# Performance work log

Hardware: AMD Instinct MI355X
Metric: run time of the kernel (lower is better)

Reference implementation:

```python
import jax, jax.numpy as jnp
import numpy as np

N, H, F, E, K = 4096, 512, 2048, 8, 2  # tokens, hidden, ffn(=4H), experts, top_k


def setup_inputs() -> dict:
    key = jax.random.key(0)
    ks = jax.random.split(key, 7)
    def w(k, shape, fan_in):
        return jax.random.normal(k, shape, dtype=jnp.float32) * (fan_in ** -0.5)
    return {
        "x": jax.random.normal(ks[0], (N, H), dtype=jnp.float32),
        "W_in": w(ks[1], (H, H), H),          # input_proj.weight  [out,in]
        "W_router": w(ks[2], (E, H), H),      # router.gate.weight [E,H]
        "W_gate": w(ks[3], (E, F, H), H),     # per-expert gate_proj.weight
        "W_up": w(ks[4], (E, F, H), H),       # per-expert up_proj.weight
        "W_down": w(ks[5], (E, H, F), F),     # per-expert down_proj.weight
        "W_out": w(ks[6], (H, H), H),         # output_proj.weight
    }


def reference(x, W_in, W_router, W_gate, W_up, W_down, W_out):
    h = x @ W_in.T                                  # [N,H] input_proj
    logits = h @ W_router.T                         # [N,E]
    # route_mode='balanced' and world_size==1 -> expert_bias is None
    probs = jax.nn.softmax(logits, axis=-1)
    top_w, top_i = jax.lax.top_k(probs, K)          # [N,K]
    top_w = jax.nn.softmax(top_w, axis=-1)          # renormalize over top-k

    # per-token combine weight for each expert: [N,E]
    onehot = jax.nn.one_hot(top_i, E, dtype=h.dtype)      # [N,K,E]
    combine_w = jnp.einsum('nk,nke->ne', top_w, onehot)

    def expert(wg, wu, wd):
        # SwiGLU FFN: down( silu(gate(h)) * up(h) )
        return (jax.nn.silu(h @ wg.T) * (h @ wu.T)) @ wd.T  # [N,H]

    expert_out = jax.vmap(expert)(W_gate, W_up, W_down)     # [E,N,H]
    combined = jnp.einsum('ne,enh->nh', combine_w, expert_out)
    return combined @ W_out.T                                # output_proj
```

## Files before the change

kernel.cpp:

```cpp
#include <hip/hip_runtime.h>

typedef unsigned short u16;
typedef unsigned int u32;
typedef short bf16x8 __attribute__((ext_vector_type(8)));
typedef float f32x4 __attribute__((ext_vector_type(4)));

#define AS1 __attribute__((address_space(1)))
#define AS3 __attribute__((address_space(3)))

#define NTOK 4096
#define HDIM 512
#define FDIM 2048
#define NEXP 8
#define NASSIGN (NTOK * 2)
#define NPAD (NASSIGN + NEXP * 128)
#define RBMAX 128

__device__ __forceinline__ void g2l16(const void* g, void* l) {
  __builtin_amdgcn_global_load_lds((const AS1 u32*)g, (AS3 u32*)l, 16, 0, 0);
}
__device__ __forceinline__ u16 f2bf(float f) {
  u32 u = __float_as_uint(f);
  u = (u + 0x7FFFu + ((u >> 16) & 1u)) >> 16;
  return (u16)u;
}
__device__ __forceinline__ float bf2f(u16 h) { return __uint_as_float(((u32)h) << 16); }

#define WAITV6() asm volatile("s_waitcnt vmcnt(6)" ::: "memory")
#define WAITV4() asm volatile("s_waitcnt vmcnt(4)" ::: "memory")
#define WAITV0() asm volatile("s_waitcnt vmcnt(0)" ::: "memory")
#define BAR() __builtin_amdgcn_s_barrier()
#define VMBAR() do { WAITV0(); BAR(); } while (0)

__global__ __launch_bounds__(256) void cvtall_kernel(
    const float* __restrict__ x, const float* __restrict__ Wi, const float* __restrict__ Wo,
    const float* __restrict__ Wg, const float* __restrict__ Wu, const float* __restrict__ Wd,
    u16* __restrict__ xb, u16* __restrict__ Wib, u16* __restrict__ Wob,
    u16* __restrict__ Wgb, u16* __restrict__ Wub, u16* __restrict__ Wdb) {
  const int gid = blockIdx.x * 256 + threadIdx.x;
  const int S = 6784 * 256;
#pragma unroll
  for (int k = 0; k < 4; ++k) {
    const int i = gid + k * S;
    const float* s; u16* d; int o;
    if (i < 524288) { s = x; d = xb; o = i; }
    else if (i < 589824) { s = Wi; d = Wib; o = i - 524288; }
    else if (i < 655360) { s = Wo; d = Wob; o = i - 589824; }
    else if (i < 2752512) { s = Wg; d = Wgb; o = i - 655360; }
    else if (i < 4849664) { s = Wu; d = Wub; o = i - 2752512; }
    else { s = Wd; d = Wdb; o = i - 4849664; }
    const float4 v = ((const float4*)s)[o];
    ushort4 t; t.x = f2bf(v.x); t.y = f2bf(v.y); t.z = f2bf(v.z); t.w = f2bf(v.w);
    ((ushort4*)d)[o] = t;
  }
}

__global__ __launch_bounds__(256) void wreff_kernel(
    const float* __restrict__ Wr, const float* __restrict__ Wi, double* __restrict__ wre) {
  const int t = blockIdx.x * 256 + threadIdx.x;
  const int e = t >> 9, k = t & 511;
  const float* wr = Wr + e * HDIM;
  double a = 0.0;
  for (int j = 0; j < HDIM; j += 8) {
#pragma unroll
    for (int u = 0; u < 8; ++u) a += (double)wr[j + u] * (double)Wi[(j + u) * HDIM + k];
  }
  wre[t] = a;
}

__global__ __launch_bounds__(256) void router_kernel(
    const float* __restrict__ x, const double* __restrict__ wre,
    int* __restrict__ idx, float* __restrict__ wts) {
  __shared__ double lw[NEXP * HDIM];
  for (int i = threadIdx.x; i < NEXP * HDIM; i += 256) lw[i] = wre[i];
  __syncthreads();
  const int n = blockIdx.x * 256 + threadIdx.x;
  const float* xr = x + (size_t)n * HDIM;
  double acc[NEXP] = {};
  for (int k4 = 0; k4 < HDIM / 4; ++k4) {
    const float4 xv = ((const float4*)xr)[k4];
    const float xc[4] = {xv.x, xv.y, xv.z, xv.w};
#pragma unroll
    for (int c = 0; c < 4; ++c) {
      const double xd = (double)xc[c];
#pragma unroll
      for (int e = 0; e < NEXP; ++e) acc[e] += xd * lw[e * HDIM + k4 * 4 + c];
    }
  }
  double mx = acc[0];
#pragma unroll
  for (int e = 1; e < NEXP; ++e) mx = acc[e] > mx ? acc[e] : mx;
  double p[NEXP], se = 0.0;
#pragma unroll
  for (int e = 0; e < NEXP; ++e) { p[e] = exp(acc[e] - mx); se += p[e]; }
  const double inv = 1.0 / se;
#pragma unroll
  for (int e = 0; e < NEXP; ++e) p[e] *= inv;
  int i0 = 0; double b0 = p[0];
#pragma unroll
  for (int e = 1; e < NEXP; ++e) if (p[e] > b0) { b0 = p[e]; i0 = e; }
  int i1 = -1; double b1 = -1.0;
#pragma unroll
  for (int e = 0; e < NEXP; ++e) if (e != i0 && p[e] > b1) { b1 = p[e]; i1 = e; }
  const double e0 = exp(b0), e1 = exp(b1);
  idx[2 * n] = i0; idx[2 * n + 1] = i1;
  wts[2 * n] = (float)(e0 / (e0 + e1));
  wts[2 * n + 1] = (float)(e1 / (e0 + e1));
}

__global__ void assign_kernel(const int* __restrict__ idx, int* __restrict__ tok,
                              int* __restrict__ pos, int* __restrict__ rbe,
                              int* __restrict__ rbp, int* __restrict__ nrb) {
  __shared__ int cnt[NEXP], cur[NEXP];
  const int tid = threadIdx.x;
  if (tid < NEXP) cnt[tid] = 0;
  __syncthreads();
  for (int a = tid; a < NASSIGN; a += 256) atomicAdd(&cnt[idx[a]], 1);
  __syncthreads();
  if (tid == 0) {
    int o = 0, n = 0;
    for (int e = 0; e < NEXP; ++e) {
      cur[e] = o;
      const int nb = (cnt[e] + 127) >> 7;
      for (int i = 0; i < nb; ++i) { rbe[n] = e; rbp[n] = o + i * 128; ++n; }
      o += nb * 128;
    }
    nrb[0] = n;
  }
  __syncthreads();
  for (int p = tid; p < NPAD; p += 256) tok[p] = 0;
  __syncthreads();
  for (int a = tid; a < NASSIGN; a += 256) {
    const int e = idx[a];
    const int q = atomicAdd(&cur[e], 1);
    tok[q] = a >> 1;
    pos[a] = q;
  }
}

template <int SB, int NT>
__device__ __forceinline__ void gemm128_body(
    const u16* __restrict__ A, const u16* __restrict__ B, void* __restrict__ C,
    int m0, int n0, int N, int K, u16* sm, int tid) {
  u16 *lA0 = sm, *lA1 = sm + 8192, *lB0 = sm + 16384, *lB1 = sm + 24576;
  const int w = tid >> 6, l = tid & 63;
  const int wm = (w >> 2) * 64, wn = (w & 3) * 32;
  const int lm = l & 15, lk = (l >> 4) * 8, xr = (l & 7) << 3;
  const int sr = l >> 3, sc = ((l & 7) ^ sr) * 8;
  const u16* As = A + (size_t)(m0 + w * 8 + sr) * K + sc;
  const u16* Bs = B + (size_t)(n0 + w * 8 + sr) * K + sc;
  f32x4 acc[4][2] = {};
  auto STG = [&](u16* dA, u16* dB, int kt) {
    g2l16(As + kt, dA + w * 512);
    g2l16(As + (size_t)64 * K + kt, dA + 4096 + w * 512);
    g2l16(Bs + kt, dB + w * 512);
    g2l16(Bs + (size_t)64 * K + kt, dB + 4096 + w * 512);
  };
  auto CMP = [&](const u16* a_, const u16* b_) {
#pragma unroll
    for (int kk = 0; kk < 2; ++kk) {
      const int ko = (kk * 32 + lk) ^ xr;
      bf16x8 af[4], bf[2];
#pragma unroll
      for (int i = 0; i < 4; ++i) af[i] = *(const bf16x8*)(a_ + (wm + i * 16 + lm) * 64 + ko);
#pragma unroll
      for (int j = 0; j < 2; ++j) bf[j] = *(const bf16x8*)(b_ + (wn + j * 16 + lm) * 64 + ko);
#pragma unroll
      for (int i = 0; i < 4; ++i)
#pragma unroll
        for (int j = 0; j < 2; ++j)
          acc[i][j] = __builtin_amdgcn_mfma_f32_16x16x32_bf16(af[i], bf[j], acc[i][j], 0, 0, 0);
    }
  };
  STG(lA0, lB0, 0);
  VMBAR();
  for (int t = 0; t < NT; t += 2) {
    if (t + 1 < NT) STG(lA1, lB1, (t + 1) * 64);
    CMP(lA0, lB0);
    VMBAR();
    if (t + 2 < NT) STG(lA0, lB0, (t + 2) * 64);
    CMP(lA1, lB1);
    VMBAR();
  }
  const int cr = (l >> 4) * 4, cc = lm;
#pragma unroll
  for (int i = 0; i < 4; ++i)
#pragma unroll
    for (int j = 0; j < 2; ++j)
#pragma unroll
      for (int r = 0; r < 4; ++r) {
        const size_t o = (size_t)(m0 + wm + i * 16 + cr + r) * N + n0 + wn + j * 16 + cc;
        if (SB) ((u16*)C)[o] = f2bf(acc[i][j][r]);
        else ((float*)C)[o] = acc[i][j][r];
      }
}

__global__ __launch_bounds__(512, 2) void ingemm_kernel(
    const u16* __restrict__ xb, const u16* __restrict__ Wib, u16* __restrict__ hb) {
  __shared__ __align__(16) u16 sm[32768];
  gemm128_body<1, 8>(xb, Wib, hb, blockIdx.y * 128, blockIdx.x * 128, HDIM, HDIM, sm, threadIdx.x);
}

__global__ __launch_bounds__(512, 2) void outgemm_kernel(
    const u16* __restrict__ cb, const u16* __restrict__ Wob, float* __restrict__ out) {
  __shared__ __align__(16) u16 sm[32768];
  gemm128_body<0, 8>(cb, Wob, out, blockIdx.y * 128, blockIdx.x * 128, HDIM, HDIM, sm, threadIdx.x);
}

__global__ __launch_bounds__(512, 2) void gateup_kernel(
    const u16* __restrict__ hb, const u16* __restrict__ Wg, const u16* __restrict__ Wu,
    u16* __restrict__ act, const int* __restrict__ tok, const int* __restrict__ rbe,
    const int* __restrict__ rbp, const int* __restrict__ nrb) {
  const int rb = blockIdx.y;
  if (rb >= nrb[0]) return;
  __shared__ __align__(16) u16 sm[73728];
  const int e = rbe[rb], p0 = rbp[rb], n0 = blockIdx.x * 128;
  const int tid = threadIdx.x, w = tid >> 6, l = tid & 63;
  const int wm = (w >> 2) * 64, wn = (w & 3) * 32;
  const int lm = l & 15, lk = (l >> 4) * 8, xr = (l & 7) << 3;
  const int sr = l >> 3, sc = ((l & 7) ^ sr) * 8;
  const u16* A0 = hb + (size_t)tok[p0 + w * 8 + sr] * HDIM + sc;
  const u16* A1 = hb + (size_t)tok[p0 + 64 + w * 8 + sr] * HDIM + sc;
  const u16* G0 = Wg + (size_t)e * FDIM * HDIM + (size_t)(n0 + w * 8 + sr) * HDIM + sc;
  const u16* G1 = G0 + (size_t)64 * HDIM;
  const u16* U0 = Wu + (size_t)e * FDIM * HDIM + (size_t)(n0 + w * 8 + sr) * HDIM + sc;
  const u16* U1 = U0 + (size_t)64 * HDIM;
  f32x4 ag[4][2] = {}, au[4][2] = {};
  auto STG = [&](int b, int kt) {
    u16* d = sm + b * 24576;
    g2l16(A0 + kt, d + w * 512);
    g2l16(A1 + kt, d + 4096 + w * 512);
    g2l16(G0 + kt, d + 8192 + w * 512);
    g2l16(G1 + kt, d + 12288 + w * 512);
    g2l16(U0 + kt, d + 16384 + w * 512);
    g2l16(U1 + kt, d + 20480 + w * 512);
  };
  auto CMP = [&](int b) {
    const u16* a_ = sm + b * 24576;
    const u16* g_ = a_ + 8192;
    const u16* u_ = a_ + 16384;
#pragma unroll
    for (int kk = 0; kk < 2; ++kk) {
      const int ko = (kk * 32 + lk) ^ xr;
      bf16x8 af[4], gf[2], uf[2];
#pragma unroll
      for (int i = 0; i < 4; ++i) af[i] = *(const bf16x8*)(a_ + (wm + i * 16 + lm) * 64 + ko);
#pragma unroll
      for (int j = 0; j < 2; ++j) {
        gf[j] = *(const bf16x8*)(g_ + (wn + j * 16 + lm) * 64 + ko);
        uf[j] = *(const bf16x8*)(u_ + (wn + j * 16 + lm) * 64 + ko);
      }
#pragma unroll
      for (int i = 0; i < 4; ++i)
#pragma unroll
        for (int j = 0; j < 2; ++j) {
          ag[i][j] = __builtin_amdgcn_mfma_f32_16x16x32_bf16(af[i], gf[j], ag[i][j], 0, 0, 0);
          au[i][j] = __builtin_amdgcn_mfma_f32_16x16x32_bf16(af[i], uf[j], au[i][j], 0, 0, 0);
        }
    }
  };
  STG(0, 0); STG(1, 64);
  WAITV6(); BAR();
#pragma unroll
  for (int t = 0; t < 8; ++t) {
    if (t + 2 < 8) STG((t + 2) % 3, (t + 2) * 64);
    CMP(t % 3);
    if (t + 2 < 8) WAITV6(); else WAITV0();
    BAR();
  }
  const int cr = (l >> 4) * 4, cc = lm;
#pragma unroll
  for (int i = 0; i < 4; ++i)
#pragma unroll
    for (int j = 0; j < 2; ++j)
#pragma unroll
      for (int r = 0; r < 4; ++r) {
        const float g = ag[i][j][r], u = au[i][j][r];
        const float s = g / (1.0f + __expf(-g));
        act[(size_t)(p0 + wm + i * 16 + cr + r) * FDIM + n0 + wn + j * 16 + cc] = f2bf(s * u);
      }
}

__global__ __launch_bounds__(512, 2) void down_kernel(
    const u16* __restrict__ act, const u16* __restrict__ Wd, u16* __restrict__ dwn,
    const int* __restrict__ rbe, const int* __restrict__ rbp, const int* __restrict__ nrb) {
  const int rb = blockIdx.y;
  if (rb >= nrb[0]) return;
  __shared__ __align__(16) u16 sm[49152];
  const int e = rbe[rb], p0 = rbp[rb], n0 = blockIdx.x * 128;
  const int tid = threadIdx.x, w = tid >> 6, l = tid & 63;
  const int g = w >> 2;
  const int wm = ((w >> 1) & 1) * 64, wn = (w & 1) * 64;
  const int lm = l & 15, lk = (l >> 4) * 8, xr = (l & 7) << 3;
  const int ko = (g * 32 + lk) ^ xr;
  const int sr = l >> 3, sc = ((l & 7) ^ sr) * 8;
  const u16* As = act + (size_t)(p0 + w * 8 + sr) * FDIM + sc;
  const u16* Bs = Wd + (size_t)e * HDIM * FDIM + (size_t)(n0 + w * 8 + sr) * FDIM + sc;
  f32x4 acc[4][4] = {};
  auto STG = [&](int b, int kt) {
    u16* d = sm + b * 16384;
    g2l16(As + kt, d + w * 512);
    g2l16(As + (size_t)64 * FDIM + kt, d + 4096 + w * 512);
    g2l16(Bs + kt, d + 8192 + w * 512);
    g2l16(Bs + (size_t)64 * FDIM + kt, d + 12288 + w * 512);
  };
  auto CMP = [&](int b) {
    const u16* a_ = sm + b * 16384;
    const u16* b_ = a_ + 8192;
    bf16x8 af[4], bf[4];
#pragma unroll
    for (int i = 0; i < 4; ++i) af[i] = *(const bf16x8*)(a_ + (wm + i * 16 + lm) * 64 + ko);
#pragma unroll
    for (int j = 0; j < 4; ++j) bf[j] = *(const bf16x8*)(b_ + (wn + j * 16 + lm) * 64 + ko);
#pragma unroll
    for (int i = 0; i < 4; ++i)
#pragma unroll
      for (int j = 0; j < 4; ++j)
        acc[i][j] = __builtin_amdgcn_mfma_f32_16x16x32_bf16(af[i], bf[j], acc[i][j], 0, 0, 0);
  };
  STG(0, 0); STG(1, 64);
  WAITV4(); BAR();
#pragma unroll
  for (int t = 0; t < 32; ++t) {
    if (t + 2 < 32) STG((t + 2) % 3, (t + 2) * 64);
    CMP(t % 3);
    if (t + 2 < 32) WAITV4(); else WAITV0();
    BAR();
  }
  asm volatile("s_waitcnt lgkmcnt(0)" ::: "memory");
  __builtin_amdgcn_sched_barrier(0);
  BAR();
  float* red = (float*)sm;
  if (g == 1) {
#pragma unroll
    for (int i = 0; i < 4; ++i)
#pragma unroll
      for (int j = 0; j < 4; ++j)
        *(f32x4*)&red[(w & 3) * 4096 + (i * 4 + j) * 256 + l * 4] = acc[i][j];
  }
  BAR();
  if (g == 0) {
    const int cr = (l >> 4) * 4, cc = lm;
#pragma unroll
    for (int i = 0; i < 4; ++i)
#pragma unroll
      for (int j = 0; j < 4; ++j) {
        const f32x4 o = *(const f32x4*)&red[w * 4096 + (i * 4 + j) * 256 + l * 4];
        const f32x4 s = acc[i][j] + o;
#pragma unroll
        for (int r = 0; r < 4; ++r)
          dwn[(size_t)(p0 + wm + i * 16 + cr + r) * HDIM + n0 + wn + j * 16 + cc] = f2bf(s[r]);
      }
  }
}

__global__ void combine_kernel(const u16* __restrict__ dwn, const int* __restrict__ pos,
                               const float* __restrict__ wts, u16* __restrict__ cb) {
  const int n = blockIdx.x, t = threadIdx.x;
  const int p0 = pos[2 * n], p1 = pos[2 * n + 1];
  const float w0 = wts[2 * n], w1 = wts[2 * n + 1];
  const ushort4 a = ((const ushort4*)(dwn + (size_t)p0 * HDIM))[t];
  const ushort4 b = ((const ushort4*)(dwn + (size_t)p1 * HDIM))[t];
  ushort4 o;
  o.x = f2bf(w0 * bf2f(a.x) + w1 * bf2f(b.x));
  o.y = f2bf(w0 * bf2f(a.y) + w1 * bf2f(b.y));
  o.z = f2bf(w0 * bf2f(a.z) + w1 * bf2f(b.z));
  o.w = f2bf(w0 * bf2f(a.w) + w1 * bf2f(b.w));
  ((ushort4*)(cb + (size_t)n * HDIM))[t] = o;
}

extern "C" void kernel_launch(void* const* d_in, const int* in_sizes, int n_in,
                              void* d_out, int out_size, void* d_ws, size_t ws_size,
                              hipStream_t stream) {
  const float* x  = (const float*)d_in[0];
  const float* Wi = (const float*)d_in[1];
  const float* Wr = (const float*)d_in[2];
  const float* Wg = (const float*)d_in[3];
  const float* Wu = (const float*)d_in[4];
  const float* Wd = (const float*)d_in[5];
  const float* Wo = (const float*)d_in[6];
  float* out = (float*)d_out;

  char* ws = (char*)d_ws;
  size_t off = 0;
  auto alloc = [&](size_t bytes) -> void* {
    off = (off + 255) & ~(size_t)255;
    void* p = ws + off;
    off += bytes;
    return p;
  };
  u16* xb  = (u16*)alloc((size_t)NTOK * HDIM * 2);
  u16* hb  = (u16*)alloc((size_t)NTOK * HDIM * 2);
  u16* cb  = (u16*)alloc((size_t)NTOK * HDIM * 2);
  u16* Wib = (u16*)alloc((size_t)HDIM * HDIM * 2);
  u16* Wob = (u16*)alloc((size_t)HDIM * HDIM * 2);
  u16* Wgb = (u16*)alloc((size_t)NEXP * FDIM * HDIM * 2);
  u16* Wub = (u16*)alloc((size_t)NEXP * FDIM * HDIM * 2);
  u16* Wdb = (u16*)alloc((size_t)NEXP * HDIM * FDIM * 2);
  u16* actb = (u16*)alloc((size_t)NPAD * FDIM * 2);
  u16* dwn = (u16*)alloc((size_t)NPAD * HDIM * 2);
  double* wre = (double*)alloc((size_t)NEXP * HDIM * 8);
  int* idx = (int*)alloc((size_t)NASSIGN * 4);
  float* wts = (float*)alloc((size_t)NASSIGN * 4);
  int* tok = (int*)alloc((size_t)NPAD * 4);
  int* pos = (int*)alloc((size_t)NASSIGN * 4);
  int* rbe = (int*)alloc((size_t)RBMAX * 4);
  int* rbp = (int*)alloc((size_t)RBMAX * 4);
  int* nrb = (int*)alloc(256);

  cvtall_kernel<<<6784, 256, 0, stream>>>(x, Wi, Wo, Wg, Wu, Wd, xb, Wib, Wob, Wgb, Wub, Wdb);
  wreff_kernel<<<16, 256, 0, stream>>>(Wr, Wi, wre);
  router_kernel<<<16, 256, 0, stream>>>(x, wre, idx, wts);
  assign_kernel<<<1, 256, 0, stream>>>(idx, tok, pos, rbe, rbp, nrb);
  ingemm_kernel<<<dim3(4, 32), 512, 0, stream>>>(xb, Wib, hb);
  gateup_kernel<<<dim3(16, 72), 512, 0, stream>>>(hb, Wgb, Wub, actb, tok, rbe, rbp, nrb);
  down_kernel<<<dim3(4, 72), 512, 0, stream>>>(actb, Wdb, dwn, rbe, rbp, nrb);
  combine_kernel<<<NTOK, 128, 0, stream>>>(dwn, pos, wts, cb);
  outgemm_kernel<<<dim3(4, 32), 512, 0, stream>>>(cb, Wob, out);
}
```

Baseline: 218.2 us.

## Fuse combine into output GEMM, restructure conversion, tune router and wreff

```diff
diff --git a/kernel.cpp b/kernel.cpp
--- a/kernel.cpp
+++ b/kernel.cpp
@@ -1,4 +1,5 @@
 #include <hip/hip_runtime.h>
+#include <hip/hip_bf16.h>
 
 typedef unsigned short u16;
 typedef unsigned int u32;
@@ -25,11 +26,28 @@
   return (u16)u;
 }
 __device__ __forceinline__ float bf2f(u16 h) { return __uint_as_float(((u32)h) << 16); }
+__device__ __forceinline__ u32 pkbf(float a, float b) {
+  __hip_bfloat162 h = __float22bfloat162_rn(float2{a, b});
+  u32 r;
+  __builtin_memcpy(&r, &h, 4);
+  return r;
+}
+__device__ __forceinline__ int4 pk8(const float4 a, const float4 b) {
+  int4 r;
+  r.x = (int)pkbf(a.x, a.y); r.y = (int)pkbf(a.z, a.w);
+  r.z = (int)pkbf(b.x, b.y); r.w = (int)pkbf(b.z, b.w);
+  return r;
+}
 
 #define WAITV6() asm volatile("s_waitcnt vmcnt(6)" ::: "memory")
 #define WAITV4() asm volatile("s_waitcnt vmcnt(4)" ::: "memory")
+#define WAITV2() asm volatile("s_waitcnt vmcnt(2)" ::: "memory")
 #define WAITV0() asm volatile("s_waitcnt vmcnt(0)" ::: "memory")
+#define LGKM0() asm volatile("s_waitcnt lgkmcnt(0)" ::: "memory")
 #define BAR() __builtin_amdgcn_s_barrier()
+#define SCB() __builtin_amdgcn_sched_barrier(0)
+#define PRIO1() __builtin_amdgcn_s_setprio(1)
+#define PRIO0() __builtin_amdgcn_s_setprio(0)
 #define VMBAR() do { WAITV0(); BAR(); } while (0)
 
 __global__ __launch_bounds__(256) void cvtall_kernel(
@@ -37,22 +55,26 @@
     const float* __restrict__ Wg, const float* __restrict__ Wu, const float* __restrict__ Wd,
     u16* __restrict__ xb, u16* __restrict__ Wib, u16* __restrict__ Wob,
     u16* __restrict__ Wgb, u16* __restrict__ Wub, u16* __restrict__ Wdb) {
-  const int gid = blockIdx.x * 256 + threadIdx.x;
-  const int S = 6784 * 256;
-#pragma unroll
-  for (int k = 0; k < 4; ++k) {
-    const int i = gid + k * S;
-    const float* s; u16* d; int o;
-    if (i < 524288) { s = x; d = xb; o = i; }
-    else if (i < 589824) { s = Wi; d = Wib; o = i - 524288; }
-    else if (i < 655360) { s = Wo; d = Wob; o = i - 589824; }
-    else if (i < 2752512) { s = Wg; d = Wgb; o = i - 655360; }
-    else if (i < 4849664) { s = Wu; d = Wub; o = i - 2752512; }
-    else { s = Wd; d = Wdb; o = i - 4849664; }
-    const float4 v = ((const float4*)s)[o];
-    ushort4 t; t.x = f2bf(v.x); t.y = f2bf(v.y); t.z = f2bf(v.z); t.w = f2bf(v.w);
-    ((ushort4*)d)[o] = t;
-  }
+  const int c = blockIdx.x, tid = threadIdx.x;
+  const float* s; u16* d; int cs;
+  if (c < 128) { s = x; d = xb; cs = 0; }
+  else if (c < 144) { s = Wi; d = Wib; cs = 128; }
+  else if (c < 160) { s = Wo; d = Wob; cs = 144; }
+  else if (c < 672) { s = Wg; d = Wgb; cs = 160; }
+  else if (c < 1184) { s = Wu; d = Wub; cs = 672; }
+  else { s = Wd; d = Wdb; cs = 1184; }
+  const size_t base = (size_t)(c - cs) * 16384 + (size_t)tid * 8;
+  const float* sp = s + base;
+  u16* dp = d + base;
+  float4 a[16];
+#pragma unroll
+  for (int j = 0; j < 8; ++j) {
+    a[2 * j] = *(const float4*)(sp + j * 2048);
+    a[2 * j + 1] = *(const float4*)(sp + j * 2048 + 4);
+  }
+#pragma unroll
+  for (int j = 0; j < 8; ++j)
+    *(int4*)(dp + j * 2048) = pk8(a[2 * j], a[2 * j + 1]);
 }
 
 __global__ __launch_bounds__(256) void wreff_kernel(
@@ -60,21 +82,23 @@
   const int t = blockIdx.x * 256 + threadIdx.x;
   const int e = t >> 9, k = t & 511;
   const float* wr = Wr + e * HDIM;
-  double a = 0.0;
-  for (int j = 0; j < HDIM; j += 8) {
-#pragma unroll
-    for (int u = 0; u < 8; ++u) a += (double)wr[j + u] * (double)Wi[(j + u) * HDIM + k];
-  }
-  wre[t] = a;
-}
-
-__global__ __launch_bounds__(256) void router_kernel(
+  double a0 = 0.0, a1 = 0.0, a2 = 0.0, a3 = 0.0;
+  for (int j = 0; j < HDIM; j += 4) {
+    a0 += (double)wr[j + 0] * (double)Wi[(j + 0) * HDIM + k];
+    a1 += (double)wr[j + 1] * (double)Wi[(j + 1) * HDIM + k];
+    a2 += (double)wr[j + 2] * (double)Wi[(j + 2) * HDIM + k];
+    a3 += (double)wr[j + 3] * (double)Wi[(j + 3) * HDIM + k];
+  }
+  wre[t] = (a0 + a1) + (a2 + a3);
+}
+
+__global__ __launch_bounds__(128) void router_kernel(
     const float* __restrict__ x, const double* __restrict__ wre,
     int* __restrict__ idx, float* __restrict__ wts) {
   __shared__ double lw[NEXP * HDIM];
-  for (int i = threadIdx.x; i < NEXP * HDIM; i += 256) lw[i] = wre[i];
+  for (int i = threadIdx.x; i < NEXP * HDIM; i += 128) lw[i] = wre[i];
   __syncthreads();
-  const int n = blockIdx.x * 256 + threadIdx.x;
+  const int n = blockIdx.x * 128 + threadIdx.x;
   const float* xr = x + (size_t)n * HDIM;
   double acc[NEXP] = {};
   for (int k4 = 0; k4 < HDIM / 4; ++k4) {
@@ -165,11 +189,13 @@
       for (int i = 0; i < 4; ++i) af[i] = *(const bf16x8*)(a_ + (wm + i * 16 + lm) * 64 + ko);
 #pragma unroll
       for (int j = 0; j < 2; ++j) bf[j] = *(const bf16x8*)(b_ + (wn + j * 16 + lm) * 64 + ko);
+      PRIO1();
 #pragma unroll
       for (int i = 0; i < 4; ++i)
 #pragma unroll
         for (int j = 0; j < 2; ++j)
           acc[i][j] = __builtin_amdgcn_mfma_f32_16x16x32_bf16(af[i], bf[j], acc[i][j], 0, 0, 0);
+      PRIO0();
     }
   };
   STG(lA0, lB0, 0);
@@ -202,9 +228,82 @@
 }
 
 __global__ __launch_bounds__(512, 2) void outgemm_kernel(
-    const u16* __restrict__ cb, const u16* __restrict__ Wob, float* __restrict__ out) {
+    const u16* __restrict__ dwn, const u16* __restrict__ Wob, const int* __restrict__ pos,
+    const float* __restrict__ wts, float* __restrict__ out) {
   __shared__ __align__(16) u16 sm[32768];
-  gemm128_body<0, 8>(cb, Wob, out, blockIdx.y * 128, blockIdx.x * 128, HDIM, HDIM, sm, threadIdx.x);
+  const int m0 = blockIdx.y * 128, n0 = blockIdx.x * 128;
+  const int tid = threadIdx.x, w = tid >> 6, l = tid & 63;
+  const int wm = (w >> 2) * 64, wn = (w & 3) * 32;
+  const int lm = l & 15, lk = (l >> 4) * 8, xr = (l & 7) << 3;
+  const int lr = l >> 3, c8 = l & 7;
+  const int sc = (c8 ^ lr) * 8;
+  const int t0 = m0 + w * 8 + lr, t1 = t0 + 64;
+  const int p00 = pos[2 * t0], p01 = pos[2 * t0 + 1];
+  const int p10 = pos[2 * t1], p11 = pos[2 * t1 + 1];
+  const float w00 = wts[2 * t0], w01 = wts[2 * t0 + 1];
+  const float w10 = wts[2 * t1], w11 = wts[2 * t1 + 1];
+  const u16* A00 = dwn + (size_t)p00 * HDIM + c8 * 8;
+  const u16* A01 = dwn + (size_t)p01 * HDIM + c8 * 8;
+  const u16* A10 = dwn + (size_t)p10 * HDIM + c8 * 8;
+  const u16* A11 = dwn + (size_t)p11 * HDIM + c8 * 8;
+  const u16* Bs = Wob + (size_t)(n0 + w * 8 + lr) * HDIM + sc;
+  f32x4 acc[4][2] = {};
+  bf16x8 a00, a01, a10, a11;
+  auto ALOAD = [&](int kt) {
+    a00 = *(const bf16x8*)(A00 + kt); a01 = *(const bf16x8*)(A01 + kt);
+    a10 = *(const bf16x8*)(A10 + kt); a11 = *(const bf16x8*)(A11 + kt);
+  };
+  auto AWRITE = [&](u16* st) {
+    bf16x8 r0, r1;
+#pragma unroll
+    for (int q = 0; q < 8; ++q) {
+      r0[q] = (short)f2bf(w00 * bf2f((u16)a00[q]) + w01 * bf2f((u16)a01[q]));
+      r1[q] = (short)f2bf(w10 * bf2f((u16)a10[q]) + w11 * bf2f((u16)a11[q]));
+    }
+    *(bf16x8*)(st + (w * 8 + lr) * 64 + sc) = r0;
+    *(bf16x8*)(st + (64 + w * 8 + lr) * 64 + sc) = r1;
+  };
+  auto STGB = [&](u16* st, int kt) {
+    g2l16(Bs + kt, st + 8192 + w * 512);
+    g2l16(Bs + (size_t)64 * HDIM + kt, st + 8192 + 4096 + w * 512);
+  };
+  auto CMP = [&](const u16* a_, const u16* b_) {
+#pragma unroll
+    for (int kk = 0; kk < 2; ++kk) {
+      const int ko = (kk * 32 + lk) ^ xr;
+      bf16x8 af[4], bf[2];
+#pragma unroll
+      for (int i = 0; i < 4; ++i) af[i] = *(const bf16x8*)(a_ + (wm + i * 16 + lm) * 64 + ko);
+#pragma unroll
+      for (int j = 0; j < 2; ++j) bf[j] = *(const bf16x8*)(b_ + (wn + j * 16 + lm) * 64 + ko);
+      PRIO1();
+#pragma unroll
+      for (int i = 0; i < 4; ++i)
+#pragma unroll
+        for (int j = 0; j < 2; ++j)
+          acc[i][j] = __builtin_amdgcn_mfma_f32_16x16x32_bf16(af[i], bf[j], acc[i][j], 0, 0, 0);
+      PRIO0();
+    }
+  };
+  ALOAD(0); SCB(); STGB(sm, 0);
+  WAITV2(); AWRITE(sm);
+  WAITV0(); LGKM0(); BAR(); SCB();
+  for (int t = 0; t < 8; ++t) {
+    u16* bu = sm + (t & 1) * 16384;
+    u16* bn = sm + ((t + 1) & 1) * 16384;
+    if (t < 7) { ALOAD((t + 1) * 64); SCB(); STGB(bn, (t + 1) * 64); }
+    CMP(bu, bu + 8192);
+    if (t < 7) { WAITV2(); AWRITE(bn); WAITV0(); }
+    LGKM0(); BAR(); SCB();
+  }
+  const int cr = (l >> 4) * 4, cc = lm;
+#pragma unroll
+  for (int i = 0; i < 4; ++i)
+#pragma unroll
+    for (int j = 0; j < 2; ++j)
+#pragma unroll
+      for (int r = 0; r < 4; ++r)
+        out[(size_t)(m0 + wm + i * 16 + cr + r) * HDIM + n0 + wn + j * 16 + cc] = acc[i][j][r];
 }
 
 __global__ __launch_bounds__(512, 2) void gateup_kernel(
@@ -327,8 +426,8 @@
     if (t + 2 < 32) WAITV4(); else WAITV0();
     BAR();
   }
-  asm volatile("s_waitcnt lgkmcnt(0)" ::: "memory");
-  __builtin_amdgcn_sched_barrier(0);
+  LGKM0();
+  SCB();
   BAR();
   float* red = (float*)sm;
   if (g == 1) {
@@ -352,21 +451,6 @@
           dwn[(size_t)(p0 + wm + i * 16 + cr + r) * HDIM + n0 + wn + j * 16 + cc] = f2bf(s[r]);
       }
   }
-}
-
-__global__ void combine_kernel(const u16* __restrict__ dwn, const int* __restrict__ pos,
-                               const float* __restrict__ wts, u16* __restrict__ cb) {
-  const int n = blockIdx.x, t = threadIdx.x;
-  const int p0 = pos[2 * n], p1 = pos[2 * n + 1];
-  const float w0 = wts[2 * n], w1 = wts[2 * n + 1];
-  const ushort4 a = ((const ushort4*)(dwn + (size_t)p0 * HDIM))[t];
-  const ushort4 b = ((const ushort4*)(dwn + (size_t)p1 * HDIM))[t];
-  ushort4 o;
-  o.x = f2bf(w0 * bf2f(a.x) + w1 * bf2f(b.x));
-  o.y = f2bf(w0 * bf2f(a.y) + w1 * bf2f(b.y));
-  o.z = f2bf(w0 * bf2f(a.z) + w1 * bf2f(b.z));
-  o.w = f2bf(w0 * bf2f(a.w) + w1 * bf2f(b.w));
-  ((ushort4*)(cb + (size_t)n * HDIM))[t] = o;
 }
 
 extern "C" void kernel_launch(void* const* d_in, const int* in_sizes, int n_in,
@@ -389,16 +473,15 @@
     off += bytes;
     return p;
   };
-  u16* xb  = (u16*)alloc((size_t)NTOK * HDIM * 2);
-  u16* hb  = (u16*)alloc((size_t)NTOK * HDIM * 2);
-  u16* cb  = (u16*)alloc((size_t)NTOK * HDIM * 2);
-  u16* Wib = (u16*)alloc((size_t)HDIM * HDIM * 2);
-  u16* Wob = (u16*)alloc((size_t)HDIM * HDIM * 2);
-  u16* Wgb = (u16*)alloc((size_t)NEXP * FDIM * HDIM * 2);
-  u16* Wub = (u16*)alloc((size_t)NEXP * FDIM * HDIM * 2);
-  u16* Wdb = (u16*)alloc((size_t)NEXP * HDIM * FDIM * 2);
+  u16* xb   = (u16*)alloc((size_t)NTOK * HDIM * 2);
+  u16* hb   = (u16*)alloc((size_t)NTOK * HDIM * 2);
+  u16* Wib  = (u16*)alloc((size_t)HDIM * HDIM * 2);
+  u16* Wob  = (u16*)alloc((size_t)HDIM * HDIM * 2);
+  u16* Wgb  = (u16*)alloc((size_t)NEXP * FDIM * HDIM * 2);
+  u16* Wub  = (u16*)alloc((size_t)NEXP * FDIM * HDIM * 2);
+  u16* Wdb  = (u16*)alloc((size_t)NEXP * HDIM * FDIM * 2);
   u16* actb = (u16*)alloc((size_t)NPAD * FDIM * 2);
-  u16* dwn = (u16*)alloc((size_t)NPAD * HDIM * 2);
+  u16* dwn  = (u16*)alloc((size_t)NPAD * HDIM * 2);
   double* wre = (double*)alloc((size_t)NEXP * HDIM * 8);
   int* idx = (int*)alloc((size_t)NASSIGN * 4);
   float* wts = (float*)alloc((size_t)NASSIGN * 4);
@@ -408,13 +491,12 @@
   int* rbp = (int*)alloc((size_t)RBMAX * 4);
   int* nrb = (int*)alloc(256);
 
-  cvtall_kernel<<<6784, 256, 0, stream>>>(x, Wi, Wo, Wg, Wu, Wd, xb, Wib, Wob, Wgb, Wub, Wdb);
+  cvtall_kernel<<<1696, 256, 0, stream>>>(x, Wi, Wo, Wg, Wu, Wd, xb, Wib, Wob, Wgb, Wub, Wdb);
   wreff_kernel<<<16, 256, 0, stream>>>(Wr, Wi, wre);
-  router_kernel<<<16, 256, 0, stream>>>(x, wre, idx, wts);
+  router_kernel<<<32, 128, 0, stream>>>(x, wre, idx, wts);
   assign_kernel<<<1, 256, 0, stream>>>(idx, tok, pos, rbe, rbp, nrb);
   ingemm_kernel<<<dim3(4, 32), 512, 0, stream>>>(xb, Wib, hb);
   gateup_kernel<<<dim3(16, 72), 512, 0, stream>>>(hb, Wgb, Wub, actb, tok, rbe, rbp, nrb);
   down_kernel<<<dim3(4, 72), 512, 0, stream>>>(actb, Wdb, dwn, rbe, rbp, nrb);
-  combine_kernel<<<NTOK, 128, 0, stream>>>(dwn, pos, wts, cb);
-  outgemm_kernel<<<dim3(4, 32), 512, 0, stream>>>(cb, Wob, out);
-}
+  outgemm_kernel<<<dim3(4, 32), 512, 0, stream>>>(dwn, Wob, pos, wts, out);
+}
```

After: 226.6 us. +3.9%, slower.

## Retile GEMMs to 128x64 blocks, rework conversion, router and down kernels

Applied to the files above, without the earlier changes.

```diff
diff --git a/kernel.cpp b/kernel.cpp
--- a/kernel.cpp
+++ b/kernel.cpp
@@ -1,4 +1,5 @@
 #include <hip/hip_runtime.h>
+#include <hip/hip_bf16.h>
 
 typedef unsigned short u16;
 typedef unsigned int u32;
@@ -25,11 +26,26 @@
   return (u16)u;
 }
 __device__ __forceinline__ float bf2f(u16 h) { return __uint_as_float(((u32)h) << 16); }
+__device__ __forceinline__ u32 pkbf(float a, float b) {
+  __hip_bfloat162 h = __float22bfloat162_rn(float2{a, b});
+  u32 r;
+  __builtin_memcpy(&r, &h, 4);
+  return r;
+}
+__device__ __forceinline__ int4 pk8(const float4 a, const float4 b) {
+  int4 r;
+  r.x = (int)pkbf(a.x, a.y); r.y = (int)pkbf(a.z, a.w);
+  r.z = (int)pkbf(b.x, b.y); r.w = (int)pkbf(b.z, b.w);
+  return r;
+}
 
 #define WAITV6() asm volatile("s_waitcnt vmcnt(6)" ::: "memory")
-#define WAITV4() asm volatile("s_waitcnt vmcnt(4)" ::: "memory")
 #define WAITV0() asm volatile("s_waitcnt vmcnt(0)" ::: "memory")
+#define LGKM0() asm volatile("s_waitcnt lgkmcnt(0)" ::: "memory")
 #define BAR() __builtin_amdgcn_s_barrier()
+#define SCB() __builtin_amdgcn_sched_barrier(0)
+#define PRIO1() __builtin_amdgcn_s_setprio(1)
+#define PRIO0() __builtin_amdgcn_s_setprio(0)
 #define VMBAR() do { WAITV0(); BAR(); } while (0)
 
 __global__ __launch_bounds__(256) void cvtall_kernel(
@@ -37,22 +53,26 @@
     const float* __restrict__ Wg, const float* __restrict__ Wu, const float* __restrict__ Wd,
     u16* __restrict__ xb, u16* __restrict__ Wib, u16* __restrict__ Wob,
     u16* __restrict__ Wgb, u16* __restrict__ Wub, u16* __restrict__ Wdb) {
-  const int gid = blockIdx.x * 256 + threadIdx.x;
-  const int S = 6784 * 256;
-#pragma unroll
-  for (int k = 0; k < 4; ++k) {
-    const int i = gid + k * S;
-    const float* s; u16* d; int o;
-    if (i < 524288) { s = x; d = xb; o = i; }
-    else if (i < 589824) { s = Wi; d = Wib; o = i - 524288; }
-    else if (i < 655360) { s = Wo; d = Wob; o = i - 589824; }
-    else if (i < 2752512) { s = Wg; d = Wgb; o = i - 655360; }
-    else if (i < 4849664) { s = Wu; d = Wub; o = i - 2752512; }
-    else { s = Wd; d = Wdb; o = i - 4849664; }
-    const float4 v = ((const float4*)s)[o];
-    ushort4 t; t.x = f2bf(v.x); t.y = f2bf(v.y); t.z = f2bf(v.z); t.w = f2bf(v.w);
-    ((ushort4*)d)[o] = t;
-  }
+  const int c = blockIdx.x, tid = threadIdx.x;
+  const float* s; u16* d; int cs;
+  if (c < 128) { s = x; d = xb; cs = 0; }
+  else if (c < 144) { s = Wi; d = Wib; cs = 128; }
+  else if (c < 160) { s = Wo; d = Wob; cs = 144; }
+  else if (c < 672) { s = Wg; d = Wgb; cs = 160; }
+  else if (c < 1184) { s = Wu; d = Wub; cs = 672; }
+  else { s = Wd; d = Wdb; cs = 1184; }
+  const size_t base = (size_t)(c - cs) * 16384 + (size_t)tid * 8;
+  const float* sp = s + base;
+  u16* dp = d + base;
+  float4 a[16];
+#pragma unroll
+  for (int j = 0; j < 8; ++j) {
+    a[2 * j] = *(const float4*)(sp + j * 2048);
+    a[2 * j + 1] = *(const float4*)(sp + j * 2048 + 4);
+  }
+#pragma unroll
+  for (int j = 0; j < 8; ++j)
+    *(int4*)(dp + j * 2048) = pk8(a[2 * j], a[2 * j + 1]);
 }
 
 __global__ __launch_bounds__(256) void wreff_kernel(
@@ -60,21 +80,23 @@
   const int t = blockIdx.x * 256 + threadIdx.x;
   const int e = t >> 9, k = t & 511;
   const float* wr = Wr + e * HDIM;
-  double a = 0.0;
-  for (int j = 0; j < HDIM; j += 8) {
-#pragma unroll
-    for (int u = 0; u < 8; ++u) a += (double)wr[j + u] * (double)Wi[(j + u) * HDIM + k];
-  }
-  wre[t] = a;
-}
-
-__global__ __launch_bounds__(256) void router_kernel(
+  double a0 = 0.0, a1 = 0.0, a2 = 0.0, a3 = 0.0;
+  for (int j = 0; j < HDIM; j += 4) {
+    a0 += (double)wr[j + 0] * (double)Wi[(j + 0) * HDIM + k];
+    a1 += (double)wr[j + 1] * (double)Wi[(j + 1) * HDIM + k];
+    a2 += (double)wr[j + 2] * (double)Wi[(j + 2) * HDIM + k];
+    a3 += (double)wr[j + 3] * (double)Wi[(j + 3) * HDIM + k];
+  }
+  wre[t] = (a0 + a1) + (a2 + a3);
+}
+
+__global__ __launch_bounds__(128) void router_kernel(
     const float* __restrict__ x, const double* __restrict__ wre,
     int* __restrict__ idx, float* __restrict__ wts) {
   __shared__ double lw[NEXP * HDIM];
-  for (int i = threadIdx.x; i < NEXP * HDIM; i += 256) lw[i] = wre[i];
-  __syncthreads();
-  const int n = blockIdx.x * 256 + threadIdx.x;
+  for (int i = threadIdx.x; i < NEXP * HDIM; i += 128) lw[i] = wre[i];
+  __syncthreads();
+  const int n = blockIdx.x * 128 + threadIdx.x;
   const float* xr = x + (size_t)n * HDIM;
   double acc[NEXP] = {};
   for (int k4 = 0; k4 < HDIM / 4; ++k4) {
@@ -132,29 +154,30 @@
   __syncthreads();
   for (int a = tid; a < NASSIGN; a += 256) {
     const int e = idx[a];
-    const int q = atomicAdd(&cur[e], 1);
+    const int q = atomicAdd(&cur[a >= 0 ? e : 0], 1);
     tok[q] = a >> 1;
     pos[a] = q;
   }
 }
 
 template <int SB, int NT>
-__device__ __forceinline__ void gemm128_body(
+__device__ __forceinline__ void gemm64_body(
     const u16* __restrict__ A, const u16* __restrict__ B, void* __restrict__ C,
-    int m0, int n0, int N, int K, u16* sm, int tid) {
-  u16 *lA0 = sm, *lA1 = sm + 8192, *lB0 = sm + 16384, *lB1 = sm + 24576;
+    int n0, int N, int K, u16* sm, int tid) {
+  u16 *l0 = sm, *l1 = sm + 12288;
   const int w = tid >> 6, l = tid & 63;
-  const int wm = (w >> 2) * 64, wn = (w & 3) * 32;
+  const int wm = (w >> 1) * 64, wn = (w & 1) * 32;
   const int lm = l & 15, lk = (l >> 4) * 8, xr = (l & 7) << 3;
   const int sr = l >> 3, sc = ((l & 7) ^ sr) * 8;
-  const u16* As = A + (size_t)(m0 + w * 8 + sr) * K + sc;
+  const u16* As = A + (size_t)(w * 8 + sr) * K + sc;
   const u16* Bs = B + (size_t)(n0 + w * 8 + sr) * K + sc;
   f32x4 acc[4][2] = {};
-  auto STG = [&](u16* dA, u16* dB, int kt) {
-    g2l16(As + kt, dA + w * 512);
-    g2l16(As + (size_t)64 * K + kt, dA + 4096 + w * 512);
-    g2l16(Bs + kt, dB + w * 512);
-    g2l16(Bs + (size_t)64 * K + kt, dB + 4096 + w * 512);
+  auto STG = [&](u16* d, int kt) {
+#pragma unroll
+    for (int c = 0; c < 4; ++c) g2l16(As + (size_t)(c * 32) * K + kt, d + c * 2048 + w * 512);
+#pragma unroll
+    for (int c = 0; c < 2; ++c)
+      g2l16(Bs + (size_t)(c * 32) * K + kt, d + 8192 + c * 2048 + w * 512);
   };
   auto CMP = [&](const u16* a_, const u16* b_) {
 #pragma unroll
@@ -165,21 +188,23 @@
       for (int i = 0; i < 4; ++i) af[i] = *(const bf16x8*)(a_ + (wm + i * 16 + lm) * 64 + ko);
 #pragma unroll
       for (int j = 0; j < 2; ++j) bf[j] = *(const bf16x8*)(b_ + (wn + j * 16 + lm) * 64 + ko);
+      PRIO1();
 #pragma unroll
       for (int i = 0; i < 4; ++i)
 #pragma unroll
         for (int j = 0; j < 2; ++j)
           acc[i][j] = __builtin_amdgcn_mfma_f32_16x16x32_bf16(af[i], bf[j], acc[i][j], 0, 0, 0);
+      PRIO0();
     }
   };
-  STG(lA0, lB0, 0);
+  STG(l0, 0);
   VMBAR();
   for (int t = 0; t < NT; t += 2) {
-    if (t + 1 < NT) STG(lA1, lB1, (t + 1) * 64);
-    CMP(lA0, lB0);
+    if (t + 1 < NT) STG(l1, (t + 1) * 64);
+    CMP(l0, l0 + 8192);
     VMBAR();
-    if (t + 2 < NT) STG(lA0, lB0, (t + 2) * 64);
-    CMP(lA1, lB1);
+    if (t + 2 < NT) STG(l0, (t + 2) * 64);
+    CMP(l1, l1 + 8192);
     VMBAR();
   }
   const int cr = (l >> 4) * 4, cc = lm;
@@ -189,22 +214,37 @@
     for (int j = 0; j < 2; ++j)
 #pragma unroll
       for (int r = 0; r < 4; ++r) {
-        const size_t o = (size_t)(m0 + wm + i * 16 + cr + r) * N + n0 + wn + j * 16 + cc;
+        const size_t o = (size_t)(wm + i * 16 + cr + r) * N + n0 + wn + j * 16 + cc;
         if (SB) ((u16*)C)[o] = f2bf(acc[i][j][r]);
         else ((float*)C)[o] = acc[i][j][r];
       }
 }
 
-__global__ __launch_bounds__(512, 2) void ingemm_kernel(
+__global__ __launch_bounds__(256, 3) void ingemm_kernel(
     const u16* __restrict__ xb, const u16* __restrict__ Wib, u16* __restrict__ hb) {
-  __shared__ __align__(16) u16 sm[32768];
-  gemm128_body<1, 8>(xb, Wib, hb, blockIdx.y * 128, blockIdx.x * 128, HDIM, HDIM, sm, threadIdx.x);
-}
-
-__global__ __launch_bounds__(512, 2) void outgemm_kernel(
+  __shared__ __align__(16) u16 sm[24576];
+  const int m0 = blockIdx.y * 128;
+  gemm64_body<1, 8>(xb + (size_t)m0 * HDIM, Wib, hb + (size_t)m0 * HDIM,
+                    blockIdx.x * 64, HDIM, HDIM, sm, threadIdx.x);
+}
+
+__global__ __launch_bounds__(256, 3) void outgemm_kernel(
     const u16* __restrict__ cb, const u16* __restrict__ Wob, float* __restrict__ out) {
-  __shared__ __align__(16) u16 sm[32768];
-  gemm128_body<0, 8>(cb, Wob, out, blockIdx.y * 128, blockIdx.x * 128, HDIM, HDIM, sm, threadIdx.x);
+  __shared__ __align__(16) u16 sm[24576];
+  const int m0 = blockIdx.y * 128;
+  gemm64_body<0, 8>(cb + (size_t)m0 * HDIM, Wob, out + (size_t)m0 * HDIM,
+                    blockIdx.x * 64, HDIM, HDIM, sm, threadIdx.x);
+}
+
+__global__ __launch_bounds__(256, 3) void down_kernel(
+    const u16* __restrict__ act, const u16* __restrict__ Wd, u16* __restrict__ dwn,
+    const int* __restrict__ rbe, const int* __restrict__ rbp, const int* __restrict__ nrb) {
+  const int rb = blockIdx.y;
+  if (rb >= nrb[0]) return;
+  __shared__ __align__(16) u16 sm[24576];
+  const int e = rbe[rb], p0 = rbp[rb];
+  gemm64_body<1, 32>(act + (size_t)p0 * FDIM, Wd + (size_t)e * HDIM * FDIM,
+                     dwn + (size_t)p0 * HDIM, blockIdx.x * 64, HDIM, FDIM, sm, threadIdx.x);
 }
 
 __global__ __launch_bounds__(512, 2) void gateup_kernel(
@@ -281,79 +321,6 @@
       }
 }
 
-__global__ __launch_bounds__(512, 2) void down_kernel(
-    const u16* __restrict__ act, const u16* __restrict__ Wd, u16* __restrict__ dwn,
-    const int* __restrict__ rbe, const int* __restrict__ rbp, const int* __restrict__ nrb) {
-  const int rb = blockIdx.y;
-  if (rb >= nrb[0]) return;
-  __shared__ __align__(16) u16 sm[49152];
-  const int e = rbe[rb], p0 = rbp[rb], n0 = blockIdx.x * 128;
-  const int tid = threadIdx.x, w = tid >> 6, l = tid & 63;
-  const int g = w >> 2;
-  const int wm = ((w >> 1) & 1) * 64, wn = (w & 1) * 64;
-  const int lm = l & 15, lk = (l >> 4) * 8, xr = (l & 7) << 3;
-  const int ko = (g * 32 + lk) ^ xr;
-  const int sr = l >> 3, sc = ((l & 7) ^ sr) * 8;
-  const u16* As = act + (size_t)(p0 + w * 8 + sr) * FDIM + sc;
-  const u16* Bs = Wd + (size_t)e * HDIM * FDIM + (size_t)(n0 + w * 8 + sr) * FDIM + sc;
-  f32x4 acc[4][4] = {};
-  auto STG = [&](int b, int kt) {
-    u16* d = sm + b * 16384;
-    g2l16(As + kt, d + w * 512);
-    g2l16(As + (size_t)64 * FDIM + kt, d + 4096 + w * 512);
-    g2l16(Bs + kt, d + 8192 + w * 512);
-    g2l16(Bs + (size_t)64 * FDIM + kt, d + 12288 + w * 512);
-  };
-  auto CMP = [&](int b) {
-    const u16* a_ = sm + b * 16384;
-    const u16* b_ = a_ + 8192;
-    bf16x8 af[4], bf[4];
-#pragma unroll
-    for (int i = 0; i < 4; ++i) af[i] = *(const bf16x8*)(a_ + (wm + i * 16 + lm) * 64 + ko);
-#pragma unroll
-    for (int j = 0; j < 4; ++j) bf[j] = *(const bf16x8*)(b_ + (wn + j * 16 + lm) * 64 + ko);
-#pragma unroll
-    for (int i = 0; i < 4; ++i)
-#pragma unroll
-      for (int j = 0; j < 4; ++j)
-        acc[i][j] = __builtin_amdgcn_mfma_f32_16x16x32_bf16(af[i], bf[j], acc[i][j], 0, 0, 0);
-  };
-  STG(0, 0); STG(1, 64);
-  WAITV4(); BAR();
-#pragma unroll
-  for (int t = 0; t < 32; ++t) {
-    if (t + 2 < 32) STG((t + 2) % 3, (t + 2) * 64);
-    CMP(t % 3);
-    if (t + 2 < 32) WAITV4(); else WAITV0();
-    BAR();
-  }
-  asm volatile("s_waitcnt lgkmcnt(0)" ::: "memory");
-  __builtin_amdgcn_sched_barrier(0);
-  BAR();
-  float* red = (float*)sm;
-  if (g == 1) {
-#pragma unroll
-    for (int i = 0; i < 4; ++i)
-#pragma unroll
-      for (int j = 0; j < 4; ++j)
-        *(f32x4*)&red[(w & 3) * 4096 + (i * 4 + j) * 256 + l * 4] = acc[i][j];
-  }
-  BAR();
-  if (g == 0) {
-    const int cr = (l >> 4) * 4, cc = lm;
-#pragma unroll
-    for (int i = 0; i < 4; ++i)
-#pragma unroll
-      for (int j = 0; j < 4; ++j) {
-        const f32x4 o = *(const f32x4*)&red[w * 4096 + (i * 4 + j) * 256 + l * 4];
-        const f32x4 s = acc[i][j] + o;
-#pragma unroll
-        for (int r = 0; r < 4; ++r)
-          dwn[(size_t)(p0 + wm + i * 16 + cr + r) * HDIM + n0 + wn + j * 16 + cc] = f2bf(s[r]);
-      }
-  }
-}
-
 __global__ void combine_kernel(const u16* __restrict__ dwn, const int* __restrict__ pos,
                                const float* __restrict__ wts, u16* __restrict__ cb) {
   const int n = blockIdx.x, t = threadIdx.x;
@@ -389,16 +356,16 @@
     off += bytes;
     return p;
   };
-  u16* xb  = (u16*)alloc((size_t)NTOK * HDIM * 2);
-  u16* hb  = (u16*)alloc((size_t)NTOK * HDIM * 2);
-  u16* cb  = (u16*)alloc((size_t)NTOK * HDIM * 2);
-  u16* Wib = (u16*)alloc((size_t)HDIM * HDIM * 2);
-  u16* Wob = (u16*)alloc((size_t)HDIM * HDIM * 2);
-  u16* Wgb = (u16*)alloc((size_t)NEXP * FDIM * HDIM * 2);
-  u16* Wub = (u16*)alloc((size_t)NEXP * FDIM * HDIM * 2);
-  u16* Wdb = (u16*)alloc((size_t)NEXP * HDIM * FDIM * 2);
+  u16* xb   = (u16*)alloc((size_t)NTOK * HDIM * 2);
+  u16* hb   = (u16*)alloc((size_t)NTOK * HDIM * 2);
+  u16* cb   = (u16*)alloc((size_t)NTOK * HDIM * 2);
+  u16* Wib  = (u16*)alloc((size_t)HDIM * HDIM * 2);
+  u16* Wob  = (u16*)alloc((size_t)HDIM * HDIM * 2);
+  u16* Wgb  = (u16*)alloc((size_t)NEXP * FDIM * HDIM * 2);
+  u16* Wub  = (u16*)alloc((size_t)NEXP * FDIM * HDIM * 2);
+  u16* Wdb  = (u16*)alloc((size_t)NEXP * HDIM * FDIM * 2);
   u16* actb = (u16*)alloc((size_t)NPAD * FDIM * 2);
-  u16* dwn = (u16*)alloc((size_t)NPAD * HDIM * 2);
+  u16* dwn  = (u16*)alloc((size_t)NPAD * HDIM * 2);
   double* wre = (double*)alloc((size_t)NEXP * HDIM * 8);
   int* idx = (int*)alloc((size_t)NASSIGN * 4);
   float* wts = (float*)alloc((size_t)NASSIGN * 4);
@@ -408,13 +375,13 @@
   int* rbp = (int*)alloc((size_t)RBMAX * 4);
   int* nrb = (int*)alloc(256);
 
-  cvtall_kernel<<<6784, 256, 0, stream>>>(x, Wi, Wo, Wg, Wu, Wd, xb, Wib, Wob, Wgb, Wub, Wdb);
+  cvtall_kernel<<<1696, 256, 0, stream>>>(x, Wi, Wo, Wg, Wu, Wd, xb, Wib, Wob, Wgb, Wub, Wdb);
   wreff_kernel<<<16, 256, 0, stream>>>(Wr, Wi, wre);
-  router_kernel<<<16, 256, 0, stream>>>(x, wre, idx, wts);
+  router_kernel<<<32, 128, 0, stream>>>(x, wre, idx, wts);
   assign_kernel<<<1, 256, 0, stream>>>(idx, tok, pos, rbe, rbp, nrb);
-  ingemm_kernel<<<dim3(4, 32), 512, 0, stream>>>(xb, Wib, hb);
+  ingemm_kernel<<<dim3(8, 32), 256, 0, stream>>>(xb, Wib, hb);
   gateup_kernel<<<dim3(16, 72), 512, 0, stream>>>(hb, Wgb, Wub, actb, tok, rbe, rbp, nrb);
-  down_kernel<<<dim3(4, 72), 512, 0, stream>>>(actb, Wdb, dwn, rbe, rbp, nrb);
+  down_kernel<<<dim3(8, 72), 256, 0, stream>>>(actb, Wdb, dwn, rbe, rbp, nrb);
   combine_kernel<<<NTOK, 128, 0, stream>>>(dwn, pos, wts, cb);
-  outgemm_kernel<<<dim3(4, 32), 512, 0, stream>>>(cb, Wob, out);
-}
+  outgemm_kernel<<<dim3(8, 32), 256, 0, stream>>>(cb, Wob, out);
+}
```

New measurement: 235.4 us. 7.9% more time.
